# Performance work log

Hardware: AMD Instinct MI355X
Metric: run time of the kernel (lower is better)

## Reference

```python
import jax, jax.numpy as jnp
import numpy as np

B, PRE, NEXT, DIN, DOUT = 256, 64, 32, 128, 64


def _squash(x):
    # x: [..., D]; scale = |x|^2/(1+|x|^2) * x/|x|
    s2 = jnp.sum(x * x, axis=-1, keepdims=True)
    return (s2 / (1.0 + s2)) * x / jnp.sqrt(s2 + 1e-8)


def setup_inputs() -> dict:
    key = jax.random.key(0)
    kx, kw = jax.random.split(key)
    x = jax.random.normal(kx, (B, PRE, DIN), dtype=jnp.float32)
    W = jax.random.normal(kw, (PRE, NEXT, DIN, DOUT), dtype=jnp.float32)
    return {"x": x, "W": W, "iter_time": 3}


def reference(x, W, iter_time):
    Bn = x.shape[0]
    k, K, _, D = W.shape
    # pose predictions: [B, k, K, D]
    p = jnp.einsum('bkd,kKdD->bkKD', x, W)
    b = jnp.zeros((Bn, k, K), dtype=x.dtype)
    q = jnp.zeros((Bn, K, D), dtype=x.dtype)
    for _ in range(iter_time):
        c = jax.nn.softmax(b, axis=-1)                 # [B,k,K]
        q = _squash(jnp.einsum('bkKD,bkK->bKD', p, c))  # [B,K,D]
        b = b + jnp.einsum('bkKD,bKD->bkK', p, q)
    return q.reshape(Bn, -1)
```

## Files before the change

### kernel.cpp

```cpp
#include <hip/hip_runtime.h>
#include <math.h>

#define BATCH 256
#define PRE   64
#define NEXT  32
#define DIN   128
#define DOUT  64

typedef __attribute__((ext_vector_type(8))) short bf16x8;
typedef __attribute__((ext_vector_type(4))) float f32x4;

__device__ __forceinline__ unsigned short f2bf(float f) {
    unsigned u = __float_as_uint(f);
    unsigned r = (u + 0x7fffu + ((u >> 16) & 1u)) >> 16;
    return (unsigned short)r;
}
__device__ __forceinline__ float bf2f(unsigned short h) {
    return __uint_as_float(((unsigned)h) << 16);
}

#define WFRAG_S 10

__global__ __launch_bounds__(256, 2) void gemm_kernel(const float* __restrict__ x,
                                                      const float* __restrict__ W,
                                                      float* __restrict__ p,
                                                      int b0)
{
    __shared__ float xs[128 * 40];
    __shared__ unsigned wpk[256 * WFRAG_S];
    const int K    = blockIdx.x;
    const int kk   = blockIdx.y;
    const int bt   = blockIdx.z;
    const int t    = threadIdx.x;
    const int wave = t >> 6;
    const int lane = t & 63;
    const int ln   = lane & 15;
    const int quad = lane >> 4;
    const int row0 = bt * 128 + wave * 32;

    f32x4 acc[2][4];
#pragma unroll
    for (int mt = 0; mt < 2; ++mt)
#pragma unroll
        for (int nt = 0; nt < 4; ++nt) acc[mt][nt] = (f32x4){0.f, 0.f, 0.f, 0.f};

    const float* Wk = W + (size_t)(kk * NEXT + K) * DIN * DOUT;

    for (int dc = 0; dc < 4; ++dc) {
        __syncthreads();
#pragma unroll
        for (int i = 0; i < 4; ++i) {
            const int f   = t + 256 * i;
            const int row = f >> 3;
            const int d4  = f & 7;
            float4 v = *(const float4*)(x + ((size_t)(b0 + bt * 128 + row) * PRE + kk) * DIN + dc * 32 + d4 * 4);
            *(float4*)&xs[row * 40 + d4 * 4] = v;
        }
#pragma unroll
        for (int it = 0; it < 8; ++it) {
            const int e  = it * 256 + t;
            const int dl = e >> 6;
            const int D  = e & 63;
            float v = Wk[(size_t)(dc * 32 + dl) * DOUT + D];
            unsigned short h = f2bf(v);
            unsigned short l = f2bf(v - bf2f(h));
            const int fr = ((D >> 4) * 64 + (dl >> 3) * 16 + (D & 15));
            wpk[fr * WFRAG_S + (dl & 7)] = (unsigned)h | ((unsigned)l << 16);
        }
        __syncthreads();

        bf16x8 ah[2], al[2];
#pragma unroll
        for (int mt = 0; mt < 2; ++mt) {
            const float* xa = &xs[(wave * 32 + mt * 16 + ln) * 40 + quad * 8];
            float4 v0 = *(const float4*)xa;
            float4 v1 = *(const float4*)(xa + 4);
            float xv[8] = {v0.x, v0.y, v0.z, v0.w, v1.x, v1.y, v1.z, v1.w};
#pragma unroll
            for (int j = 0; j < 8; ++j) {
                unsigned short h = f2bf(xv[j]);
                ah[mt][j] = (short)h;
                al[mt][j] = (short)f2bf(xv[j] - bf2f(h));
            }
        }
        bf16x8 bh[4], bl[4];
#pragma unroll
        for (int nt = 0; nt < 4; ++nt) {
            const unsigned* wp = &wpk[(nt * 64 + quad * 16 + ln) * WFRAG_S];
            unsigned pk[8];
#pragma unroll
            for (int i2 = 0; i2 < 4; ++i2) *(uint2*)&pk[i2 * 2] = *(const uint2*)&wp[i2 * 2];
            union { bf16x8 v; unsigned u[4]; } BH, BL;
#pragma unroll
            for (int i2 = 0; i2 < 4; ++i2) {
                BH.u[i2] = (pk[2 * i2] & 0xffffu) | (pk[2 * i2 + 1] << 16);
                BL.u[i2] = (pk[2 * i2] >> 16) | (pk[2 * i2 + 1] & 0xffff0000u);
            }
            bh[nt] = BH.v; bl[nt] = BL.v;
        }
#pragma unroll
        for (int mt = 0; mt < 2; ++mt)
#pragma unroll
            for (int nt = 0; nt < 4; ++nt) {
                acc[mt][nt] = __builtin_amdgcn_mfma_f32_16x16x32_bf16(ah[mt], bh[nt], acc[mt][nt], 0, 0, 0);
                acc[mt][nt] = __builtin_amdgcn_mfma_f32_16x16x32_bf16(al[mt], bh[nt], acc[mt][nt], 0, 0, 0);
                acc[mt][nt] = __builtin_amdgcn_mfma_f32_16x16x32_bf16(ah[mt], bl[nt], acc[mt][nt], 0, 0, 0);
            }
    }

#pragma unroll
    for (int mt = 0; mt < 2; ++mt)
#pragma unroll
        for (int nt = 0; nt < 4; ++nt) {
            const int D = nt * 16 + ln;
#pragma unroll
            for (int r = 0; r < 4; ++r) {
                const int row = row0 + mt * 16 + quad * 4 + r;
                p[((size_t)(row * PRE + kk) * NEXT + K) * DOUT + D] = acc[mt][nt][r];
            }
        }
}

__global__ __launch_bounds__(512, 1) void route_kernel(const float* __restrict__ p,
                                                       float* __restrict__ out,
                                                       int b0)
{
    __shared__ float qpart[8 * 2048];
    __shared__ float qsum[2048];
    const int b    = blockIdx.x;
    const int t    = threadIdx.x;
    const int w    = t >> 6;
    const int lane = t & 63;
    const int g    = lane >> 4;
    const int m    = lane & 15;
    const float4* pb = (const float4*)(p + (size_t)b * (PRE * NEXT * DOUT));

    for (int idx = t; idx < 2048; idx += 512) qsum[idx] = 0.f;
    __syncthreads();

    for (int pass = 0; pass < 3; ++pass) {
        float4 qa[8];
#pragma unroll
        for (int j = 0; j < 8; ++j) qa[j] = (float4){0.f, 0.f, 0.f, 0.f};

        float4 pv[2][8];
        {
            const size_t sb = (size_t)w * 512;
#pragma unroll
            for (int j = 0; j < 8; ++j) pv[0][j] = pb[sb + j * 64 + lane];
        }
#pragma unroll
        for (int i = 0; i < 8; ++i) {
            const int buf = i & 1;
            if (i < 7) {
                const size_t sb = (size_t)((i + 1) * 8 + w) * 512;
#pragma unroll
                for (int j = 0; j < 8; ++j) pv[buf ^ 1][j] = pb[sb + j * 64 + lane];
            }
            float c[8];
            if (pass == 0) {
#pragma unroll
                for (int j = 0; j < 8; ++j) c[j] = 1.0f / 32.0f;
            } else {
#pragma unroll
                for (int j = 0; j < 8; ++j) {
                    float4 qv = *(const float4*)&qsum[(j * 4 + g) * 64 + m * 4];
                    float d = pv[buf][j].x * qv.x + pv[buf][j].y * qv.y
                            + pv[buf][j].z * qv.z + pv[buf][j].w * qv.w;
                    d += __shfl_xor(d, 1);
                    d += __shfl_xor(d, 2);
                    d += __shfl_xor(d, 4);
                    d += __shfl_xor(d, 8);
                    c[j] = d;
                }
                float mx = c[0];
#pragma unroll
                for (int j = 1; j < 8; ++j) mx = fmaxf(mx, c[j]);
                mx = fmaxf(mx, __shfl_xor(mx, 16));
                mx = fmaxf(mx, __shfl_xor(mx, 32));
                float s = 0.f;
#pragma unroll
                for (int j = 0; j < 8; ++j) { c[j] = __expf(c[j] - mx); s += c[j]; }
                s += __shfl_xor(s, 16);
                s += __shfl_xor(s, 32);
                float inv = 1.0f / s;
#pragma unroll
                for (int j = 0; j < 8; ++j) c[j] *= inv;
            }
#pragma unroll
            for (int j = 0; j < 8; ++j) {
                qa[j].x += c[j] * pv[buf][j].x;
                qa[j].y += c[j] * pv[buf][j].y;
                qa[j].z += c[j] * pv[buf][j].z;
                qa[j].w += c[j] * pv[buf][j].w;
            }
        }
#pragma unroll
        for (int j = 0; j < 8; ++j)
            *(float4*)&qpart[w * 2048 + (j * 4 + g) * 64 + m * 4] = qa[j];
        __syncthreads();

        {
            const int Kq = t >> 4, ch = t & 15;
            float4 v = (float4){0.f, 0.f, 0.f, 0.f};
#pragma unroll
            for (int ww = 0; ww < 8; ++ww) {
                float4 s4 = *(const float4*)&qpart[ww * 2048 + Kq * 64 + ch * 4];
                v.x += s4.x; v.y += s4.y; v.z += s4.z; v.w += s4.w;
            }
            float s2 = v.x * v.x + v.y * v.y + v.z * v.z + v.w * v.w;
            s2 += __shfl_xor(s2, 1);
            s2 += __shfl_xor(s2, 2);
            s2 += __shfl_xor(s2, 4);
            s2 += __shfl_xor(s2, 8);
            float fsc = s2 / ((1.f + s2) * sqrtf(s2 + 1e-8f));
            v.x *= fsc; v.y *= fsc; v.z *= fsc; v.w *= fsc;
            if (pass < 2) {
                float* qd = &qsum[Kq * 64 + ch * 4];
                qd[0] += v.x; qd[1] += v.y; qd[2] += v.z; qd[3] += v.w;
            } else {
                *(float4*)(out + (size_t)(b0 + b) * 2048 + Kq * 64 + ch * 4) = v;
            }
        }
        if (pass < 2) __syncthreads();
    }
}

extern "C" void kernel_launch(void* const* d_in, const int* in_sizes, int n_in,
                              void* d_out, int out_size, void* d_ws, size_t ws_size,
                              hipStream_t stream) {
    const float* x = (const float*)d_in[0];
    const float* W = (const float*)d_in[1];
    float* out = (float*)d_out;
    float* p   = (float*)d_ws;

    const int chunk = (ws_size >= (size_t)134217728) ? 256 : 128;

    for (int b0 = 0; b0 < BATCH; b0 += chunk) {
        gemm_kernel<<<dim3(NEXT, PRE, chunk / 128), 256, 0, stream>>>(x, W, p, b0);
        route_kernel<<<chunk, 512, 0, stream>>>(p, out, b0);
    }
}
```

Measured before the change: 271.4 us.

## Double route kernel threads to 1024 and pad shared q buffers

The routing kernel now runs 16 waves per batch element instead of 8, each handling 4 instead of 8 input-capsule groups, so each wave has fewer serial loads per pass. Partial q sums from the extra waves are folded into the first 8 waves' buffers through an extra synchronised pass. Shared q rows are padded to a stride of 68 to reduce LDS bank conflicts. The squash step now uses 2 elements per thread over 32 lanes. The cost is an additional barrier and more register pressure under a 1024-thread launch bound.

```diff
diff --git a/kernel.cpp b/kernel.cpp
--- a/kernel.cpp
+++ b/kernel.cpp
@@ -121,12 +121,15 @@
         }
 }
 
-__global__ __launch_bounds__(512, 1) void route_kernel(const float* __restrict__ p,
-                                                       float* __restrict__ out,
-                                                       int b0)
+#define QSTR 68
+#define QBUF (32 * QSTR)
+
+__global__ __launch_bounds__(1024, 1) void route_kernel(const float* __restrict__ p,
+                                                        float* __restrict__ out,
+                                                        int b0)
 {
-    __shared__ float qpart[8 * 2048];
-    __shared__ float qsum[2048];
+    __shared__ float qpart[8 * QBUF];
+    __shared__ float qsum[QBUF];
     const int b    = blockIdx.x;
     const int t    = threadIdx.x;
     const int w    = t >> 6;
@@ -135,7 +138,7 @@
     const int m    = lane & 15;
     const float4* pb = (const float4*)(p + (size_t)b * (PRE * NEXT * DOUT));
 
-    for (int idx = t; idx < 2048; idx += 512) qsum[idx] = 0.f;
+    for (int idx = t; idx < QBUF; idx += 1024) qsum[idx] = 0.f;
     __syncthreads();
 
     for (int pass = 0; pass < 3; ++pass) {
@@ -150,10 +153,10 @@
             for (int j = 0; j < 8; ++j) pv[0][j] = pb[sb + j * 64 + lane];
         }
 #pragma unroll
-        for (int i = 0; i < 8; ++i) {
+        for (int i = 0; i < 4; ++i) {
             const int buf = i & 1;
-            if (i < 7) {
-                const size_t sb = (size_t)((i + 1) * 8 + w) * 512;
+            if (i < 3) {
+                const size_t sb = (size_t)((i + 1) * 16 + w) * 512;
 #pragma unroll
                 for (int j = 0; j < 8; ++j) pv[buf ^ 1][j] = pb[sb + j * 64 + lane];
             }
@@ -164,7 +167,7 @@
             } else {
 #pragma unroll
                 for (int j = 0; j < 8; ++j) {
-                    float4 qv = *(const float4*)&qsum[(j * 4 + g) * 64 + m * 4];
+                    float4 qv = *(const float4*)&qsum[(j * 4 + g) * QSTR + m * 4];
                     float d = pv[buf][j].x * qv.x + pv[buf][j].y * qv.y
                             + pv[buf][j].z * qv.z + pv[buf][j].w * qv.w;
                     d += __shfl_xor(d, 1);
@@ -195,31 +198,45 @@
                 qa[j].w += c[j] * pv[buf][j].w;
             }
         }
-#pragma unroll
-        for (int j = 0; j < 8; ++j)
-            *(float4*)&qpart[w * 2048 + (j * 4 + g) * 64 + m * 4] = qa[j];
+        if (w < 8) {
+#pragma unroll
+            for (int j = 0; j < 8; ++j)
+                *(float4*)&qpart[w * QBUF + (j * 4 + g) * QSTR + m * 4] = qa[j];
+        }
+        __syncthreads();
+        if (w >= 8) {
+#pragma unroll
+            for (int j = 0; j < 8; ++j) {
+                float* qd = &qpart[(w - 8) * QBUF + (j * 4 + g) * QSTR + m * 4];
+                float4 old = *(const float4*)qd;
+                old.x += qa[j].x; old.y += qa[j].y; old.z += qa[j].z; old.w += qa[j].w;
+                *(float4*)qd = old;
+            }
+        }
         __syncthreads();
 
         {
-            const int Kq = t >> 4, ch = t & 15;
-            float4 v = (float4){0.f, 0.f, 0.f, 0.f};
+            const int Kq = t >> 5, pr = t & 31;
+            float vx = 0.f, vy = 0.f;
 #pragma unroll
             for (int ww = 0; ww < 8; ++ww) {
-                float4 s4 = *(const float4*)&qpart[ww * 2048 + Kq * 64 + ch * 4];
-                v.x += s4.x; v.y += s4.y; v.z += s4.z; v.w += s4.w;
-            }
-            float s2 = v.x * v.x + v.y * v.y + v.z * v.z + v.w * v.w;
+                const float* s2p = &qpart[ww * QBUF + Kq * QSTR + pr * 2];
+                vx += s2p[0]; vy += s2p[1];
+            }
+            float s2 = vx * vx + vy * vy;
             s2 += __shfl_xor(s2, 1);
             s2 += __shfl_xor(s2, 2);
             s2 += __shfl_xor(s2, 4);
             s2 += __shfl_xor(s2, 8);
+            s2 += __shfl_xor(s2, 16);
             float fsc = s2 / ((1.f + s2) * sqrtf(s2 + 1e-8f));
-            v.x *= fsc; v.y *= fsc; v.z *= fsc; v.w *= fsc;
+            vx *= fsc; vy *= fsc;
             if (pass < 2) {
-                float* qd = &qsum[Kq * 64 + ch * 4];
-                qd[0] += v.x; qd[1] += v.y; qd[2] += v.z; qd[3] += v.w;
+                float* qd = &qsum[Kq * QSTR + pr * 2];
+                qd[0] += vx; qd[1] += vy;
             } else {
-                *(float4*)(out + (size_t)(b0 + b) * 2048 + Kq * 64 + ch * 4) = v;
+                float* od = out + (size_t)(b0 + b) * 2048 + Kq * 64 + pr * 2;
+                od[0] = vx; od[1] = vy;
             }
         }
         if (pass < 2) __syncthreads();
@@ -238,6 +255,6 @@
 
     for (int b0 = 0; b0 < BATCH; b0 += chunk) {
         gemm_kernel<<<dim3(NEXT, PRE, chunk / 128), 256, 0, stream>>>(x, W, p, b0);
-        route_kernel<<<chunk, 512, 0, stream>>>(p, out, b0);
+        route_kernel<<<chunk, 1024, 0, stream>>>(p, out, b0);
     }
 }
```

Result: faster. 251.1 us (-7.5%).

## Stage routing pose rows into LDS via direct global-to-LDS async loads

Applied to the files above, without the earlier changes.

The routing kernel now loads each wave's pose rows with global_load_lds into double-buffered per-wave LDS slots instead of register double-buffering. Manual vmcnt/lgkmcnt waits overlap the fetch of the next row with compute on the current one. The partial-q reduction buffer reuses the staging area and the q arrays are padded to a stride of 68 to cut LDS bank conflicts. This raises LDS use to about 137KB and relies on hand-written waitcnt sequencing, which could be fragile.

```diff
diff --git a/kernel.cpp b/kernel.cpp
--- a/kernel.cpp
+++ b/kernel.cpp
@@ -121,21 +121,39 @@
         }
 }
 
+#define QSTR 68
+#define QBUF (32 * QSTR)
+#define SLOTF 2048
+
+typedef const __attribute__((address_space(1))) unsigned g_u32;
+typedef __attribute__((address_space(3))) unsigned lds_u32;
+
+__device__ __forceinline__ void stage_row(const float* gp, float* slot, int lane) {
+    const float* gl = gp + lane * 4;
+#pragma unroll
+    for (int i = 0; i < 8; ++i) {
+        __builtin_amdgcn_global_load_lds((g_u32*)(gl + i * 256),
+                                         (lds_u32*)(slot + i * 256), 16, 0, 0);
+    }
+}
+
 __global__ __launch_bounds__(512, 1) void route_kernel(const float* __restrict__ p,
                                                        float* __restrict__ out,
                                                        int b0)
 {
-    __shared__ float qpart[8 * 2048];
-    __shared__ float qsum[2048];
+    __shared__ float stage[8 * 2 * SLOTF];
+    __shared__ float qsum[QBUF];
     const int b    = blockIdx.x;
     const int t    = threadIdx.x;
     const int w    = t >> 6;
     const int lane = t & 63;
     const int g    = lane >> 4;
     const int m    = lane & 15;
-    const float4* pb = (const float4*)(p + (size_t)b * (PRE * NEXT * DOUT));
-
-    for (int idx = t; idx < 2048; idx += 512) qsum[idx] = 0.f;
+    const float* pb = p + (size_t)b * (PRE * NEXT * DOUT);
+    float* const myslot0 = &stage[(w * 2 + 0) * SLOTF];
+    float* const myslot1 = &stage[(w * 2 + 1) * SLOTF];
+
+    for (int idx = t; idx < QBUF; idx += 512) qsum[idx] = 0.f;
     __syncthreads();
 
     for (int pass = 0; pass < 3; ++pass) {
@@ -143,61 +161,70 @@
 #pragma unroll
         for (int j = 0; j < 8; ++j) qa[j] = (float4){0.f, 0.f, 0.f, 0.f};
 
-        float4 pv[2][8];
-        {
-            const size_t sb = (size_t)w * 512;
-#pragma unroll
-            for (int j = 0; j < 8; ++j) pv[0][j] = pb[sb + j * 64 + lane];
-        }
-#pragma unroll
-        for (int i = 0; i < 8; ++i) {
-            const int buf = i & 1;
-            if (i < 7) {
-                const size_t sb = (size_t)((i + 1) * 8 + w) * 512;
-#pragma unroll
-                for (int j = 0; j < 8; ++j) pv[buf ^ 1][j] = pb[sb + j * 64 + lane];
-            }
-            float c[8];
+        stage_row(pb + (size_t)w * SLOTF, myslot0, lane);
+        stage_row(pb + (size_t)(8 + w) * SLOTF, myslot1, lane);
+
+#pragma unroll
+        for (int c = 0; c < 8; ++c) {
+            if (c < 7) asm volatile("s_waitcnt vmcnt(8)" ::: "memory");
+            else       asm volatile("s_waitcnt vmcnt(0)" ::: "memory");
+
+            float* slot = (c & 1) ? myslot1 : myslot0;
+            float4 pf[8];
+#pragma unroll
+            for (int j = 0; j < 8; ++j)
+                pf[j] = *(const float4*)(slot + j * 256 + lane * 4);
+            asm volatile("s_waitcnt lgkmcnt(0)" ::: "memory");
+            if (c < 6)
+                stage_row(pb + (size_t)((c + 2) * 8 + w) * SLOTF, slot, lane);
+            __builtin_amdgcn_sched_barrier(0);
+
+            float c8[8];
             if (pass == 0) {
 #pragma unroll
-                for (int j = 0; j < 8; ++j) c[j] = 1.0f / 32.0f;
+                for (int j = 0; j < 8; ++j) c8[j] = 1.0f / 32.0f;
             } else {
 #pragma unroll
                 for (int j = 0; j < 8; ++j) {
-                    float4 qv = *(const float4*)&qsum[(j * 4 + g) * 64 + m * 4];
-                    float d = pv[buf][j].x * qv.x + pv[buf][j].y * qv.y
-                            + pv[buf][j].z * qv.z + pv[buf][j].w * qv.w;
+                    float4 qv = *(const float4*)&qsum[(j * 4 + g) * QSTR + m * 4];
+                    float d = pf[j].x * qv.x + pf[j].y * qv.y
+                            + pf[j].z * qv.z + pf[j].w * qv.w;
                     d += __shfl_xor(d, 1);
                     d += __shfl_xor(d, 2);
                     d += __shfl_xor(d, 4);
                     d += __shfl_xor(d, 8);
-                    c[j] = d;
+                    c8[j] = d;
                 }
-                float mx = c[0];
-#pragma unroll
-                for (int j = 1; j < 8; ++j) mx = fmaxf(mx, c[j]);
+                float mx = c8[0];
+#pragma unroll
+                for (int j = 1; j < 8; ++j) mx = fmaxf(mx, c8[j]);
                 mx = fmaxf(mx, __shfl_xor(mx, 16));
                 mx = fmaxf(mx, __shfl_xor(mx, 32));
                 float s = 0.f;
 #pragma unroll
-                for (int j = 0; j < 8; ++j) { c[j] = __expf(c[j] - mx); s += c[j]; }
+                for (int j = 0; j < 8; ++j) { c8[j] = __expf(c8[j] - mx); s += c8[j]; }
                 s += __shfl_xor(s, 16);
                 s += __shfl_xor(s, 32);
                 float inv = 1.0f / s;
 #pragma unroll
-                for (int j = 0; j < 8; ++j) c[j] *= inv;
+                for (int j = 0; j < 8; ++j) c8[j] *= inv;
             }
 #pragma unroll
             for (int j = 0; j < 8; ++j) {
-                qa[j].x += c[j] * pv[buf][j].x;
-                qa[j].y += c[j] * pv[buf][j].y;
-                qa[j].z += c[j] * pv[buf][j].z;
-                qa[j].w += c[j] * pv[buf][j].w;
-            }
-        }
-#pragma unroll
-        for (int j = 0; j < 8; ++j)
-            *(float4*)&qpart[w * 2048 + (j * 4 + g) * 64 + m * 4] = qa[j];
+                qa[j].x += c8[j] * pf[j].x;
+                qa[j].y += c8[j] * pf[j].y;
+                qa[j].z += c8[j] * pf[j].z;
+                qa[j].w += c8[j] * pf[j].w;
+            }
+        }
+
+        __syncthreads();
+        {
+            float* qp = &stage[w * QBUF];
+#pragma unroll
+            for (int j = 0; j < 8; ++j)
+                *(float4*)(qp + (j * 4 + g) * QSTR + m * 4) = qa[j];
+        }
         __syncthreads();
 
         {
@@ -205,7 +232,7 @@
             float4 v = (float4){0.f, 0.f, 0.f, 0.f};
 #pragma unroll
             for (int ww = 0; ww < 8; ++ww) {
-                float4 s4 = *(const float4*)&qpart[ww * 2048 + Kq * 64 + ch * 4];
+                float4 s4 = *(const float4*)&stage[ww * QBUF + Kq * QSTR + ch * 4];
                 v.x += s4.x; v.y += s4.y; v.z += s4.z; v.w += s4.w;
             }
             float s2 = v.x * v.x + v.y * v.y + v.z * v.z + v.w * v.w;
@@ -216,7 +243,7 @@
             float fsc = s2 / ((1.f + s2) * sqrtf(s2 + 1e-8f));
             v.x *= fsc; v.y *= fsc; v.z *= fsc; v.w *= fsc;
             if (pass < 2) {
-                float* qd = &qsum[Kq * 64 + ch * 4];
+                float* qd = &qsum[Kq * QSTR + ch * 4];
                 qd[0] += v.x; qd[1] += v.y; qd[2] += v.z; qd[3] += v.w;
             } else {
                 *(float4*)(out + (size_t)(b0 + b) * 2048 + Kq * 64 + ch * 4) = v;
```

Measured after the change: 411.2 us. +51.5%, slower.
